# Kernel optimization log

Hardware: AMD Instinct MI355X
Metric: run time of the kernel (lower is better)

## Reference

```python
import jax, jax.numpy as jnp
import numpy as np

NUM_TOTAL = 150000
NUM_USER = 50000
NUM_ITEM = NUM_TOTAL - NUM_USER
D = 128
SOC_L = 2
CO_L = 2
NEG = 10
R = 0.7
E_SOC = 1600000
E_CO = 3200000
B = 512
MAX_UI = 64
MAX_IU = 50
W = 32
HOP = 3


def _sage_lgcn(x, src, dst, w, n, layers):
    # SAGEConv with edge-softmax weights over destination (LGCN 'mean' option).
    m = jax.lax.stop_gradient(jax.ops.segment_max(w, dst, num_segments=n))
    e = jnp.exp(w - m[dst])
    s = jax.ops.segment_sum(e, dst, num_segments=n)
    alpha = e / (s[dst] + 1e-16)
    for _ in range(layers):
        x = jax.ops.segment_sum(alpha[:, None] * x[src], dst, num_segments=n)
    return x  # LGCN.forward returns the last conv output (not the averaged sum)


def _sym_lgcn(x, src, dst, n, layers):
    # LGCConv: gcn_norm with added self-loops, symmetric D^-1/2 A D^-1/2.
    loop = jnp.arange(n)
    s2 = jnp.concatenate([src, loop])
    d2 = jnp.concatenate([dst, loop])
    deg = jax.ops.segment_sum(jnp.ones_like(d2, dtype=jnp.float32), d2, num_segments=n)
    dinv = jnp.where(deg > 0, deg ** -0.5, 0.0)
    ew = dinv[s2] * dinv[d2]
    for _ in range(layers):
        x = jax.ops.segment_sum(ew[:, None] * x[s2], d2, num_segments=n)
    return x


def _l2norm(x):
    return x / jnp.maximum(jnp.linalg.norm(x, axis=-1, keepdims=True), 1e-12)


def setup_inputs() -> dict:
    ks = jax.random.split(jax.random.key(0), 10)
    id_emb = 0.1 * jax.random.normal(ks[0], (NUM_TOTAL, D), jnp.float32)
    soc_id_emb = 0.1 * jax.random.normal(ks[1], (NUM_TOTAL, D), jnp.float32)
    soc_ext_weight = jax.random.uniform(ks[2], (E_SOC,), jnp.float32)
    soc_edge_index = jax.random.randint(ks[3], (2, E_SOC), 0, NUM_TOTAL)
    co_edge_index = jax.random.randint(ks[4], (2, E_CO), 0, NUM_TOTAL)
    uid = jax.random.randint(ks[5], (B,), 0, NUM_USER)
    pi = jax.random.randint(ks[9], (B,), NUM_USER, NUM_TOTAL)
    n_id = jnp.stack([uid, pi], axis=1)
    user_items = jax.random.randint(ks[6], (B, MAX_UI), 0, NUM_ITEM)
    item_users = jax.random.randint(ks[7], (NUM_ITEM, MAX_IU), 0, NUM_USER)
    walks = jax.random.randint(ks[8], (B, W, HOP), 0, NUM_TOTAL)
    return dict(id_emb=id_emb, soc_id_emb=soc_id_emb, soc_ext_weight=soc_ext_weight,
                soc_edge_index=soc_edge_index, co_edge_index=co_edge_index, n_id=n_id,
                user_items=user_items, item_users=item_users, walks=walks)


def reference(id_emb, soc_id_emb, soc_ext_weight, soc_edge_index, co_edge_index,
              n_id, user_items, item_users, walks):
    pi_id = n_id[:, 1]
    # two message-passing stacks
    soc_emb = _sage_lgcn(soc_id_emb, soc_edge_index[0], soc_edge_index[1],
                         soc_ext_weight, NUM_TOTAL, SOC_L)
    co_emb = _sym_lgcn(id_emb, co_edge_index[0], co_edge_index[1], NUM_TOTAL, CO_L)
    zero = jnp.zeros((1, D), id_emb.dtype)
    co_pad = jnp.concatenate([co_emb, zero], 0)
    soc_pad = jnp.concatenate([soc_emb, zero], 0)
    # vectorized per-user negative sampling: exclude interacted items, sample
    # NEG without replacement via top-k over masked uniform noise.
    rows = jnp.arange(B)[:, None]
    cols = jnp.where(user_items >= 0, user_items, 0)
    avail = jnp.ones((B, NUM_ITEM), jnp.int32).at[rows, cols].min(
        (user_items < 0).astype(jnp.int32))
    noise = jax.random.uniform(jax.random.key(42), (B, NUM_ITEM))
    scorez = jnp.where(avail > 0, noise, -1.0)
    _, neg_local = jax.lax.top_k(scorez, NEG)
    cand = jnp.concatenate([pi_id[:, None], neg_local + NUM_USER], axis=1)  # [B, 1+NEG]
    # item anchor soc embedding = mean of soc_emb over interacting users
    iu_idx = jnp.where(item_users >= 0, item_users, NUM_TOTAL)  # pad -> zero row
    cnt = (item_users >= 0).sum(-1, keepdims=True).astype(id_emb.dtype) + 1e-7
    anchor = soc_pad[iu_idx].sum(1) / cnt  # [NUM_ITEM, D]
    u_ref = jnp.concatenate([soc_emb[:NUM_USER], anchor, zero], 0)  # [NUM_TOTAL+1, D]
    co_n = _l2norm(co_pad)
    soc_n = _l2norm(u_ref)
    wk = walks.reshape(B, -1)  # [B, W*HOP]
    co_sim = (jnp.einsum('bcd,bwd->bcw', co_n[cand], co_n[wk]) + 1.0) * 0.5
    soc_sim = (jnp.einsum('bcd,bwd->bcw', soc_n[cand], soc_n[wk]) + 1.0) * 0.5
    return R * co_sim.mean(-1) + (1.0 - R) * soc_sim.mean(-1)  # [B, 1+NEG]
```

## Files before the change

### kernel.cpp

```cpp
#include <hip/hip_runtime.h>
#include <hip/hip_fp16.h>
#include <stdint.h>

#define NUM_TOTAL 150000
#define NUM_USER  50000
#define NUM_ITEM  100000
#define E_SOC 1600000
#define E_CO  3200000
#define BATCH 512
#define MAX_UI 64
#define MAX_IU 50
#define NWALK 96
#define NCAND 11
#define MASKW 3125
#define NB    586
#define NWG   192

__device__ __forceinline__ uint32_t rotl32(uint32_t x, int r){ return (x<<r)|(x>>(32-r)); }

__device__ __forceinline__ void tf_core(uint32_t x0, uint32_t x1, uint32_t& o0, uint32_t& o1){
  const uint32_t k0 = 0u, k1 = 42u, k2 = 0u ^ 42u ^ 0x1BD11BDAu;
  x0 += k0; x1 += k1;
#define TF_R4(a,b,c,d) \
  x0+=x1; x1=rotl32(x1,a); x1^=x0; \
  x0+=x1; x1=rotl32(x1,b); x1^=x0; \
  x0+=x1; x1=rotl32(x1,c); x1^=x0; \
  x0+=x1; x1=rotl32(x1,d); x1^=x0;
  TF_R4(13,15,26,6)   x0+=k1; x1+=k2+1u;
  TF_R4(17,29,16,24)  x0+=k2; x1+=k0+2u;
  TF_R4(13,15,26,6)   x0+=k0; x1+=k1+3u;
  TF_R4(17,29,16,24)  x0+=k1; x1+=k2+4u;
  TF_R4(13,15,26,6)   x0+=k2; x1+=k0+5u;
#undef TF_R4
  o0 = x0; o1 = x1;
}

__device__ __forceinline__ uint32_t tf_bits(uint32_t j){
  uint32_t o0, o1;
  tf_core(0u, j, o0, o1);
  return o0 ^ o1;
}

__global__ __launch_bounds__(256) void pcount_k(const int* __restrict__ dst, int E, int chunk,
                                                int* __restrict__ cntMat ){
  __shared__ int h[NB];
  int tid = threadIdx.x, wg = blockIdx.x;
  for (int i=tid; i<NB; i+=256) h[i]=0;
  __syncthreads();
  int lo = wg*chunk, hi = lo+chunk; if (hi > E) hi = E;
  for (int i=lo+tid; i<hi; i+=256) atomicAdd(&h[dst[i]>>8], 1);
  __syncthreads();
  for (int i=tid; i<NB; i+=256) cntMat[wg*NB + i] = h[i];
}

__global__ __launch_bounds__(1024) void pscan_k(int* __restrict__ cntMat, int* __restrict__ bbase, int E){
  __shared__ int sa[1024];
  int tid = threadIdx.x;
  int tot = 0;
  if (tid < NB){
    for (int wg=0; wg<NWG; ++wg) tot += cntMat[wg*NB + tid];
  }
  sa[tid] = tot;
  __syncthreads();
  for (int s=1; s<1024; s<<=1){
    int v = (tid>=s)?sa[tid-s]:0;
    __syncthreads();
    sa[tid] += v;
    __syncthreads();
  }
  if (tid < NB){
    int base = sa[tid] - tot;
    bbase[tid] = base;
    int run = base;
    for (int wg=0; wg<NWG; ++wg){
      int c = cntMat[wg*NB + tid];
      cntMat[wg*NB + tid] = run;
      run += c;
    }
  }
  if (tid == 0) bbase[NB] = E;
}

__global__ __launch_bounds__(256) void pplace_soc_k(const int* __restrict__ src,
        const int* __restrict__ dst, const float* __restrict__ wgt,
        const int* __restrict__ offMat, unsigned long long* __restrict__ rec, int E, int chunk){
  __shared__ int curx[NB];
  int tid = threadIdx.x, wg = blockIdx.x;
  for (int i=tid; i<NB; i+=256) curx[i] = offMat[wg*NB + i];
  __syncthreads();
  int lo = wg*chunk, hi = lo+chunk; if (hi > E) hi = E;
  for (int i=lo+tid; i<hi; i+=256){
    int d = dst[i];
    int p = atomicAdd(&curx[d>>8], 1);
    rec[p] = ((unsigned long long)__float_as_uint(wgt[i])<<32)
           | (unsigned)(((d&255)<<18) | src[i]);
  }
}

__global__ __launch_bounds__(256) void pplace_co_k(const int* __restrict__ src,
        const int* __restrict__ dst, const int* __restrict__ offMat,
        unsigned int* __restrict__ rec, int E, int chunk){
  __shared__ int curx[NB];
  int tid = threadIdx.x, wg = blockIdx.x;
  for (int i=tid; i<NB; i+=256) curx[i] = offMat[wg*NB + i];
  __syncthreads();
  int lo = wg*chunk, hi = lo+chunk; if (hi > E) hi = E;
  for (int i=lo+tid; i<hi; i+=256){
    int d = dst[i];
    int p = atomicAdd(&curx[d>>8], 1);
    rec[p] = (unsigned)(((d&255)<<18) | src[i]);
  }
}

__global__ __launch_bounds__(256) void csc_soc_k(const unsigned long long* __restrict__ rec,
    const int* __restrict__ bbase, int* __restrict__ off,
    int* __restrict__ srcS, float* __restrict__ wS){
  __shared__ int cnt[256], basex[256], curx[256];
  int b = blockIdx.x, tid = threadIdx.x;
  int lo = bbase[b], hi = bbase[b+1];
  cnt[tid] = 0;
  __syncthreads();
  for (int i = lo + tid; i < hi; i += 256){
    unsigned long long r = rec[i];
    atomicAdd(&cnt[(((unsigned)r) >> 18) & 255], 1);
  }
  __syncthreads();
  int c = cnt[tid];
  basex[tid] = c; __syncthreads();
  for (int s=1; s<256; s<<=1){
    int t = (tid>=s)?basex[tid-s]:0; __syncthreads();
    basex[tid]+=t; __syncthreads();
  }
  int excl = basex[tid]-c;
  int node = b*256+tid;
  if (node <= NUM_TOTAL) off[node] = lo + excl;
  basex[tid] = excl; curx[tid] = 0;
  __syncthreads();
  for (int i = lo + tid; i < hi; i += 256){
    unsigned long long r = rec[i];
    unsigned lw = (unsigned)r;
    int dl = (lw>>18)&255;
    int p = lo + basex[dl] + atomicAdd(&curx[dl],1);
    srcS[p] = lw & 0x3FFFF;
    wS[p] = __uint_as_float((unsigned)(r>>32));
  }
}

__global__ __launch_bounds__(256) void csc_co_k(const unsigned int* __restrict__ rec,
    const int* __restrict__ bbase, int* __restrict__ off, int* __restrict__ srcS){
  __shared__ int cnt[256], basex[256], curx[256];
  int b = blockIdx.x, tid = threadIdx.x;
  int lo = bbase[b], hi = bbase[b+1];
  cnt[tid] = 0;
  __syncthreads();
  for (int i = lo + tid; i < hi; i += 256){
    unsigned r = rec[i];
    atomicAdd(&cnt[(r >> 18) & 255], 1);
  }
  __syncthreads();
  int c = cnt[tid];
  basex[tid] = c; __syncthreads();
  for (int s=1; s<256; s<<=1){
    int t = (tid>=s)?basex[tid-s]:0; __syncthreads();
    basex[tid]+=t; __syncthreads();
  }
  int excl = basex[tid]-c;
  int node = b*256+tid;
  if (node <= NUM_TOTAL) off[node] = lo + excl;
  basex[tid] = excl; curx[tid] = 0;
  __syncthreads();
  for (int i = lo + tid; i < hi; i += 256){
    unsigned r = rec[i];
    int dl = (r>>18)&255;
    int p = lo + basex[dl] + atomicAdd(&curx[dl],1);
    srcS[p] = r & 0x3FFFF;
  }
}

__global__ void dinv_k(const int* __restrict__ off, float* __restrict__ dinv, int n){
  int i = blockIdx.x*blockDim.x + threadIdx.x, st = gridDim.x*blockDim.x;
  for (; i<n; i+=st){
    int deg = off[i+1]-off[i];
    dinv[i] = 1.0f / sqrtf((float)(deg + 1));
  }
}

__global__ void alpha_k(const int* __restrict__ off, float* __restrict__ wS, int n){
  int v = blockIdx.x*blockDim.x + threadIdx.x;
  if (v >= n) return;
  int e0 = off[v], e1 = off[v+1];
  if (e0 == e1) return;
  float m = -3.402823466e+38f;
  for (int e=e0; e<e1; ++e) m = fmaxf(m, wS[e]);
  float s = 0.f;
  for (int e=e0; e<e1; ++e) s += expf(wS[e] - m);
  float inv = 1.0f / (s + 1e-16f);
  for (int e=e0; e<e1; ++e) wS[e] = expf(wS[e] - m) * inv;
}

__global__ void f2h2_k(const float4* __restrict__ a, uint2* __restrict__ oa,
                       const float4* __restrict__ b, uint2* __restrict__ ob, int n4){
  int i = blockIdx.x*blockDim.x+threadIdx.x, st = gridDim.x*blockDim.x;
  for (; i<n4; i+=st){
    float4 va = a[i], vb = b[i];
    __half2 l = __float22half2_rn(make_float2(va.x,va.y));
    __half2 h = __float22half2_rn(make_float2(va.z,va.w));
    uint2 u; u.x = *(unsigned*)&l; u.y = *(unsigned*)&h;
    oa[i] = u;
    l = __float22half2_rn(make_float2(vb.x,vb.y));
    h = __float22half2_rn(make_float2(vb.z,vb.w));
    u.x = *(unsigned*)&l; u.y = *(unsigned*)&h;
    ob[i] = u;
  }
}

__global__ void agg_soc8_k(const __half2* __restrict__ x, __half2* __restrict__ y,
                           const int* __restrict__ off, const int* __restrict__ srcS,
                           const float* __restrict__ wE, int n){
  int gw = (blockIdx.x*blockDim.x + threadIdx.x) >> 6;
  int lane = threadIdx.x & 63;
  if (gw >= n) return;
  float ax = 0.f, ay = 0.f;
  int e = off[gw], e1 = off[gw+1];
  for (; e + 8 <= e1; e += 8){
    int s0=srcS[e],s1=srcS[e+1],s2=srcS[e+2],s3=srcS[e+3];
    int s4=srcS[e+4],s5=srcS[e+5],s6=srcS[e+6],s7=srcS[e+7];
    float a0=wE[e],a1=wE[e+1],a2=wE[e+2],a3=wE[e+3];
    float a4=wE[e+4],a5=wE[e+5],a6=wE[e+6],a7=wE[e+7];
    __half2 h0=x[(size_t)s0*64+lane], h1=x[(size_t)s1*64+lane];
    __half2 h2=x[(size_t)s2*64+lane], h3=x[(size_t)s3*64+lane];
    __half2 h4=x[(size_t)s4*64+lane], h5=x[(size_t)s5*64+lane];
    __half2 h6=x[(size_t)s6*64+lane], h7=x[(size_t)s7*64+lane];
    float2 f0=__half22float2(h0), f1=__half22float2(h1), f2=__half22float2(h2), f3=__half22float2(h3);
    float2 f4=__half22float2(h4), f5=__half22float2(h5), f6=__half22float2(h6), f7=__half22float2(h7);
    ax += a0*f0.x + a1*f1.x + a2*f2.x + a3*f3.x + a4*f4.x + a5*f5.x + a6*f6.x + a7*f7.x;
    ay += a0*f0.y + a1*f1.y + a2*f2.y + a3*f3.y + a4*f4.y + a5*f5.y + a6*f6.y + a7*f7.y;
  }
  for (; e < e1; ++e){
    int s = srcS[e]; float a = wE[e];
    float2 f = __half22float2(x[(size_t)s*64 + lane]);
    ax += a*f.x; ay += a*f.y;
  }
  y[(size_t)gw*64 + lane] = __float22half2_rn(make_float2(ax, ay));
}

__global__ void agg_co8_k(const __half2* __restrict__ x, __half2* __restrict__ y,
                          const int* __restrict__ off, const int* __restrict__ srcS,
                          const float* __restrict__ dinv, int n){
  int gw = (blockIdx.x*blockDim.x + threadIdx.x) >> 6;
  int lane = threadIdx.x & 63;
  if (gw >= n) return;
  float dv = dinv[gw];
  float2 fs = __half22float2(x[(size_t)gw*64 + lane]);
  float ax = dv*dv*fs.x, ay = dv*dv*fs.y;
  int e = off[gw], e1 = off[gw+1];
  for (; e + 8 <= e1; e += 8){
    int s0=srcS[e],s1=srcS[e+1],s2=srcS[e+2],s3=srcS[e+3];
    int s4=srcS[e+4],s5=srcS[e+5],s6=srcS[e+6],s7=srcS[e+7];
    float a0=dinv[s0]*dv,a1=dinv[s1]*dv,a2=dinv[s2]*dv,a3=dinv[s3]*dv;
    float a4=dinv[s4]*dv,a5=dinv[s5]*dv,a6=dinv[s6]*dv,a7=dinv[s7]*dv;
    __half2 h0=x[(size_t)s0*64+lane], h1=x[(size_t)s1*64+lane];
    __half2 h2=x[(size_t)s2*64+lane], h3=x[(size_t)s3*64+lane];
    __half2 h4=x[(size_t)s4*64+lane], h5=x[(size_t)s5*64+lane];
    __half2 h6=x[(size_t)s6*64+lane], h7=x[(size_t)s7*64+lane];
    float2 f0=__half22float2(h0), f1=__half22float2(h1), f2=__half22float2(h2), f3=__half22float2(h3);
    float2 f4=__half22float2(h4), f5=__half22float2(h5), f6=__half22float2(h6), f7=__half22float2(h7);
    ax += a0*f0.x + a1*f1.x + a2*f2.x + a3*f3.x + a4*f4.x + a5*f5.x + a6*f6.x + a7*f7.x;
    ay += a0*f0.y + a1*f1.y + a2*f2.y + a3*f3.y + a4*f4.y + a5*f5.y + a6*f6.y + a7*f7.y;
  }
  for (; e < e1; ++e){
    int s = srcS[e]; float a = dinv[s]*dv;
    float2 f = __half22float2(x[(size_t)s*64 + lane]);
    ax += a*f.x; ay += a*f.y;
  }
  y[(size_t)gw*64 + lane] = __float22half2_rn(make_float2(ax, ay));
}

__global__ void norm_h_k(__half2* __restrict__ x, int n){
  int gw = (blockIdx.x*blockDim.x + threadIdx.x) >> 6;
  int lane = threadIdx.x & 63;
  if (gw >= n) return;
  __half2* p = x + (size_t)gw*64;
  float2 v = __half22float2(p[lane]);
  float ss = v.x*v.x + v.y*v.y;
  #pragma unroll
  for (int s=32; s; s>>=1) ss += __shfl_xor(ss, s, 64);
  float sc = 1.0f / fmaxf(sqrtf(ss), 1e-12f);
  p[lane] = __float22half2_rn(make_float2(v.x*sc, v.y*sc));
}

__global__ void anchor_h_k(const __half2* __restrict__ soc, const int* __restrict__ item_users,
                           __half2* __restrict__ outI, int n){
  int gw = (blockIdx.x*blockDim.x + threadIdx.x) >> 6;
  int lane = threadIdx.x & 63;
  if (gw >= n) return;
  const int* us = item_users + (size_t)gw*MAX_IU;
  float ax = 0.f, ay = 0.f;
  for (int k=0; k<MAX_IU; k+=10){
    int u0=us[k],u1=us[k+1],u2=us[k+2],u3=us[k+3],u4=us[k+4];
    int u5=us[k+5],u6=us[k+6],u7=us[k+7],u8=us[k+8],u9=us[k+9];
    __half2 h0=soc[(size_t)u0*64+lane], h1=soc[(size_t)u1*64+lane];
    __half2 h2=soc[(size_t)u2*64+lane], h3=soc[(size_t)u3*64+lane];
    __half2 h4=soc[(size_t)u4*64+lane], h5=soc[(size_t)u5*64+lane];
    __half2 h6=soc[(size_t)u6*64+lane], h7=soc[(size_t)u7*64+lane];
    __half2 h8=soc[(size_t)u8*64+lane], h9=soc[(size_t)u9*64+lane];
    float2 f0=__half22float2(h0), f1=__half22float2(h1), f2=__half22float2(h2);
    float2 f3=__half22float2(h3), f4=__half22float2(h4), f5=__half22float2(h5);
    float2 f6=__half22float2(h6), f7=__half22float2(h7), f8=__half22float2(h8);
    float2 f9=__half22float2(h9);
    ax += f0.x+f1.x+f2.x+f3.x+f4.x+f5.x+f6.x+f7.x+f8.x+f9.x;
    ay += f0.y+f1.y+f2.y+f3.y+f4.y+f5.y+f6.y+f7.y+f8.y+f9.y;
  }
  const float inv = 1.0f / (50.0f + 1e-7f);
  ax *= inv; ay *= inv;
  float ss = ax*ax + ay*ay;
  #pragma unroll
  for (int s=32; s; s>>=1) ss += __shfl_xor(ss, s, 64);
  float sc = 1.0f / fmaxf(sqrtf(ss), 1e-12f);
  outI[(size_t)gw*64 + lane] = __float22half2_rn(make_float2(ax*sc, ay*sc));
}

__global__ __launch_bounds__(256) void topk_k(const int* __restrict__ user_items,
                                              const int* __restrict__ n_id,
                                              int* __restrict__ cand){
  __shared__ unsigned int mask[MASKW];
  __shared__ unsigned long long pool[2560];
  __shared__ unsigned long long red[256];
  int b = blockIdx.x, tid = threadIdx.x;
  for (int i=tid; i<MASKW; i+=256) mask[i] = 0u;
  __syncthreads();
  if (tid < MAX_UI){
    int it = user_items[b*MAX_UI + tid];
    if (it >= 0) atomicOr(&mask[it>>5], 1u << (it & 31));
  }
  __syncthreads();

  unsigned long long best[10];
  #pragma unroll
  for (int k=0; k<10; ++k) best[k] = 0ull;

  unsigned int jbase = (unsigned int)b * 100000u;
  for (int i=tid; i<NUM_ITEM; i+=256){
    if ((mask[i>>5] >> (i & 31)) & 1u) continue;
    unsigned int bits = tf_bits(jbase + (unsigned int)i);
    unsigned int v = bits >> 9;
    unsigned long long key = ((unsigned long long)v << 32) | (unsigned int)(~(unsigned int)i);
    if (key > best[9]){
      best[9] = key;
      #pragma unroll
      for (int r=9; r>0; --r)
        if (best[r] > best[r-1]){ unsigned long long t = best[r-1]; best[r-1] = best[r]; best[r] = t; }
    }
  }
  #pragma unroll
  for (int k=0; k<10; ++k) pool[tid*10 + k] = best[k];
  __syncthreads();

  for (int r=0; r<10; ++r){
    unsigned long long m = 0ull;
    #pragma unroll
    for (int k=0; k<10; ++k){ unsigned long long p = pool[tid*10 + k]; if (p > m) m = p; }
    red[tid] = m; __syncthreads();
    for (int s=128; s>0; s>>=1){
      if (tid < s && red[tid+s] > red[tid]) red[tid] = red[tid+s];
      __syncthreads();
    }
    unsigned long long win = red[0];
    if (tid == 0)
      cand[b*NCAND + 1 + r] = NUM_USER + (int)(~(unsigned int)(win & 0xffffffffull));
    #pragma unroll
    for (int k=0; k<10; ++k) if (pool[tid*10 + k] == win) pool[tid*10 + k] = 0ull;
    __syncthreads();
  }
  if (tid == 0) cand[b*NCAND] = n_id[b*2 + 1];
}

__global__ void sim_h_k(const __half2* __restrict__ coN, const __half2* __restrict__ socU,
                        const __half2* __restrict__ socI, const int* __restrict__ cand,
                        const int* __restrict__ walks, float* __restrict__ out){
  int b = blockIdx.x;
  int lane = threadIdx.x;
  float scx=0.f, scy=0.f, ssx=0.f, ssy=0.f;
  for (int w=0; w<NWALK; w+=4){
    int i0 = walks[b*NWALK + w],   i1 = walks[b*NWALK + w+1];
    int i2 = walks[b*NWALK + w+2], i3 = walks[b*NWALK + w+3];
    __half2 c0 = coN[(size_t)i0*64 + lane], c1 = coN[(size_t)i1*64 + lane];
    __half2 c2 = coN[(size_t)i2*64 + lane], c3 = coN[(size_t)i3*64 + lane];
    const __half2* p0 = (i0 < NUM_USER) ? socU + (size_t)i0*64 : socI + (size_t)(i0-NUM_USER)*64;
    const __half2* p1 = (i1 < NUM_USER) ? socU + (size_t)i1*64 : socI + (size_t)(i1-NUM_USER)*64;
    const __half2* p2 = (i2 < NUM_USER) ? socU + (size_t)i2*64 : socI + (size_t)(i2-NUM_USER)*64;
    const __half2* p3 = (i3 < NUM_USER) ? socU + (size_t)i3*64 : socI + (size_t)(i3-NUM_USER)*64;
    __half2 s0 = p0[lane], s1 = p1[lane], s2 = p2[lane], s3 = p3[lane];
    float2 fc0 = __half22float2(c0), fc1 = __half22float2(c1);
    float2 fc2 = __half22float2(c2), fc3 = __half22float2(c3);
    float2 fs0 = __half22float2(s0), fs1 = __half22float2(s1);
    float2 fs2 = __half22float2(s2), fs3 = __half22float2(s3);
    scx += fc0.x + fc1.x + fc2.x + fc3.x;
    scy += fc0.y + fc1.y + fc2.y + fc3.y;
    ssx += fs0.x + fs1.x + fs2.x + fs3.x;
    ssy += fs0.y + fs1.y + fs2.y + fs3.y;
  }
  for (int c=0; c<NCAND; ++c){
    int idx = cand[b*NCAND + c];
    float2 cv = __half22float2(coN[(size_t)idx*64 + lane]);
    float2 sv = __half22float2(socI[(size_t)(idx - NUM_USER)*64 + lane]);
    float dco = cv.x*scx + cv.y*scy;
    float dso = sv.x*ssx + sv.y*ssy;
    #pragma unroll
    for (int s=32; s; s>>=1){
      dco += __shfl_xor(dco, s, 64);
      dso += __shfl_xor(dso, s, 64);
    }
    if (lane == 0){
      float com = 0.5f + 0.5f*(dco / 96.0f);
      float som = 0.5f + 0.5f*(dso / 96.0f);
      out[b*NCAND + c] = 0.7f*com + 0.3f*som;
    }
  }
}

extern "C" void kernel_launch(void* const* d_in, const int* in_sizes, int n_in,
                              void* d_out, int out_size, void* d_ws, size_t ws_size,
                              hipStream_t stream){
  (void)in_sizes; (void)n_in; (void)out_size; (void)ws_size;
  const float* id_emb     = (const float*)d_in[0];
  const float* soc_id_emb = (const float*)d_in[1];
  const float* soc_w      = (const float*)d_in[2];
  const int*   soc_ei     = (const int*)d_in[3];
  const int*   co_ei      = (const int*)d_in[4];
  const int*   n_id       = (const int*)d_in[5];
  const int*   user_items = (const int*)d_in[6];
  const int*   item_users = (const int*)d_in[7];
  const int*   walks      = (const int*)d_in[8];
  float* out = (float*)d_out;

  char* w = (char*)d_ws;
  size_t cur = 0;
  auto take = [&](size_t bytes)->void*{
    void* p = w + cur;
    cur = (cur + bytes + 255) & ~(size_t)255;
    return p;
  };
  __half2* socId16 = (__half2*)take((size_t)NUM_TOTAL*64*4);
  __half2* id16    = (__half2*)take((size_t)NUM_TOTAL*64*4);
  __half2* t16     = (__half2*)take((size_t)NUM_TOTAL*64*4);
  __half2* soc16   = (__half2*)take((size_t)NUM_TOTAL*64*4);
  __half2* co16    = (__half2*)take((size_t)NUM_TOTAL*64*4);
  int*   socOff  = (int*)take((size_t)(NUM_TOTAL+1)*4);
  int*   coOff   = (int*)take((size_t)(NUM_TOTAL+1)*4);
  float* dinv    = (float*)take((size_t)NUM_TOTAL*4);
  int*   socSrcS = (int*)take((size_t)E_SOC*4);
  float* socWS   = (float*)take((size_t)E_SOC*4);
  int*   coSrcS  = (int*)take((size_t)E_CO*4);
  int*   cntMatS = (int*)take((size_t)NWG*NB*4);
  int*   cntMatC = (int*)take((size_t)NWG*NB*4);
  int*   bbaseS  = (int*)take((size_t)(NB+1)*4);
  int*   bbaseC  = (int*)take((size_t)(NB+1)*4);
  int*   cand    = (int*)take((size_t)BATCH*NCAND*4);

  unsigned long long* recS = (unsigned long long*)t16;
  unsigned int*       recC = (unsigned int*)((char*)t16 + (size_t)E_SOC*8);

  __half2* anch16 = socId16;

  const int T = 256;
  const int chunkS = (E_SOC + NWG - 1) / NWG;
  const int chunkC = (E_CO  + NWG - 1) / NWG;

  pcount_k<<<NWG, T, 0, stream>>>(soc_ei + E_SOC, E_SOC, chunkS, cntMatS);
  pcount_k<<<NWG, T, 0, stream>>>(co_ei + E_CO,  E_CO,  chunkC, cntMatC);
  pscan_k<<<1, 1024, 0, stream>>>(cntMatS, bbaseS, E_SOC);
  pscan_k<<<1, 1024, 0, stream>>>(cntMatC, bbaseC, E_CO);
  pplace_soc_k<<<NWG, T, 0, stream>>>(soc_ei, soc_ei + E_SOC, soc_w, cntMatS, recS, E_SOC, chunkS);
  pplace_co_k <<<NWG, T, 0, stream>>>(co_ei,  co_ei  + E_CO,         cntMatC, recC, E_CO,  chunkC);
  csc_soc_k<<<NB, T, 0, stream>>>(recS, bbaseS, socOff, socSrcS, socWS);
  csc_co_k <<<NB, T, 0, stream>>>(recC, bbaseC, coOff, coSrcS);

  dinv_k<<<(NUM_TOTAL + T - 1)/T, T, 0, stream>>>(coOff, dinv, NUM_TOTAL);
  alpha_k<<<(NUM_TOTAL + T - 1)/T, T, 0, stream>>>(socOff, socWS, NUM_TOTAL);

  f2h2_k<<<2048, T, 0, stream>>>((const float4*)soc_id_emb, (uint2*)socId16,
                                 (const float4*)id_emb,     (uint2*)id16, NUM_TOTAL*32);

  int aggGrid = (NUM_TOTAL + 3) / 4;
  agg_soc8_k<<<aggGrid, T, 0, stream>>>(socId16, soc16, socOff, socSrcS, socWS, NUM_TOTAL);
  agg_soc8_k<<<aggGrid, T, 0, stream>>>(soc16,   t16,   socOff, socSrcS, socWS, NUM_TOTAL);
  agg_co8_k <<<aggGrid, T, 0, stream>>>(id16,    co16,  coOff,  coSrcS,  dinv,  NUM_TOTAL);
  agg_co8_k <<<aggGrid, T, 0, stream>>>(co16,    id16,  coOff,  coSrcS,  dinv,  NUM_TOTAL);

  __half2* socE = t16;
  __half2* coE  = id16;

  norm_h_k<<<aggGrid, T, 0, stream>>>(coE, NUM_TOTAL);
  anchor_h_k<<<(NUM_ITEM + 3)/4, T, 0, stream>>>(socE, item_users, anch16, NUM_ITEM);
  norm_h_k<<<(NUM_USER + 3)/4, T, 0, stream>>>(socE, NUM_USER);

  topk_k<<<BATCH, T, 0, stream>>>(user_items, n_id, cand);
  sim_h_k<<<BATCH, 64, 0, stream>>>(coE, socE, anch16, cand, walks, out);
}
```

Baseline: 1.155 ms.

## Split negative top-k into threshold-filter pass and small merge pass

The per-row top-10 over 100k random scores is replaced by two kernels. The first spreads each row over four blocks, keeps only candidates whose score clears a fixed threshold, and writes them to a small survivor buffer. The second selects the top 10 from those survivors. If fewer than 10 survive, it falls back to a slow full rescan, so the result stays exact. This removes the per-thread insertion sort and serial reduction over 100k items, and uses more blocks for better parallelism. The threshold is tuned to the score distribution, and the survivor cap could overflow, so it depends on the noise statistics.

```diff
diff --git a/kernel.cpp b/kernel.cpp
--- a/kernel.cpp
+++ b/kernel.cpp
@@ -12,9 +12,13 @@
 #define MAX_IU 50
 #define NWALK 96
 #define NCAND 11
-#define MASKW 3125
 #define NB    586
 #define NWG   192
+#define PARTS 4
+#define PIT   25000
+#define PMW   784
+#define SCAP  192
+#define TH    8377900u
 
 __device__ __forceinline__ uint32_t rotl32(uint32_t x, int r){ return (x<<r)|(x>>(32-r)); }
 
@@ -320,57 +324,108 @@
   outI[(size_t)gw*64 + lane] = __float22half2_rn(make_float2(ax*sc, ay*sc));
 }
 
-__global__ __launch_bounds__(256) void topk_k(const int* __restrict__ user_items,
+__global__ __launch_bounds__(256) void negA_k(const int* __restrict__ user_items,
+                                              unsigned long long* __restrict__ surv,
+                                              int* __restrict__ scnt){
+  __shared__ unsigned int mask[PMW];
+  __shared__ int lcnt;
+  int blk = blockIdx.x;
+  int row = blk >> 2, part = blk & 3;
+  int base = part * PIT;
+  int tid = threadIdx.x;
+  for (int i=tid; i<PMW; i+=256) mask[i] = 0u;
+  if (tid == 0) lcnt = 0;
+  __syncthreads();
+  if (tid < MAX_UI){
+    int it = user_items[row*MAX_UI + tid];
+    if (it >= base && it < base + PIT){
+      int li = it - base;
+      atomicOr(&mask[li>>5], 1u << (li & 31));
+    }
+  }
+  __syncthreads();
+  unsigned jbase = (unsigned)row * 100000u + (unsigned)base;
+  for (int k = tid; k < PIT; k += 512){
+    int i1 = k + 256;
+    uint32_t b0 = tf_bits(jbase + (unsigned)k);
+    uint32_t b1 = tf_bits(jbase + (unsigned)(i1 < PIT ? i1 : k));
+    uint32_t v0 = b0 >> 9;
+    uint32_t v1 = b1 >> 9;
+    if (v0 >= TH && !((mask[k>>5] >> (k&31)) & 1u)){
+      int p = atomicAdd(&lcnt, 1);
+      if (p < SCAP)
+        surv[(size_t)blk*SCAP + p] = ((unsigned long long)v0 << 32) | (unsigned)(~(unsigned)(base + k));
+    }
+    if (i1 < PIT && v1 >= TH && !((mask[i1>>5] >> (i1&31)) & 1u)){
+      int p = atomicAdd(&lcnt, 1);
+      if (p < SCAP)
+        surv[(size_t)blk*SCAP + p] = ((unsigned long long)v1 << 32) | (unsigned)(~(unsigned)(base + i1));
+    }
+  }
+  __syncthreads();
+  if (tid == 0) scnt[blk] = (lcnt < SCAP) ? lcnt : SCAP;
+}
+
+__global__ __launch_bounds__(256) void negB_k(const unsigned long long* __restrict__ surv,
+                                              const int* __restrict__ scnt,
+                                              const int* __restrict__ user_items,
                                               const int* __restrict__ n_id,
                                               int* __restrict__ cand){
-  __shared__ unsigned int mask[MASKW];
-  __shared__ unsigned long long pool[2560];
+  __shared__ unsigned long long keys[PARTS*SCAP];
   __shared__ unsigned long long red[256];
+  __shared__ int cnts[PARTS];
+  __shared__ int uix[MAX_UI];
   int b = blockIdx.x, tid = threadIdx.x;
-  for (int i=tid; i<MASKW; i+=256) mask[i] = 0u;
-  __syncthreads();
-  if (tid < MAX_UI){
-    int it = user_items[b*MAX_UI + tid];
-    if (it >= 0) atomicOr(&mask[it>>5], 1u << (it & 31));
-  }
-  __syncthreads();
-
-  unsigned long long best[10];
-  #pragma unroll
-  for (int k=0; k<10; ++k) best[k] = 0ull;
-
-  unsigned int jbase = (unsigned int)b * 100000u;
-  for (int i=tid; i<NUM_ITEM; i+=256){
-    if ((mask[i>>5] >> (i & 31)) & 1u) continue;
-    unsigned int bits = tf_bits(jbase + (unsigned int)i);
-    unsigned int v = bits >> 9;
-    unsigned long long key = ((unsigned long long)v << 32) | (unsigned int)(~(unsigned int)i);
-    if (key > best[9]){
-      best[9] = key;
-      #pragma unroll
-      for (int r=9; r>0; --r)
-        if (best[r] > best[r-1]){ unsigned long long t = best[r-1]; best[r-1] = best[r]; best[r] = t; }
-    }
-  }
-  #pragma unroll
-  for (int k=0; k<10; ++k) pool[tid*10 + k] = best[k];
-  __syncthreads();
-
-  for (int r=0; r<10; ++r){
-    unsigned long long m = 0ull;
-    #pragma unroll
-    for (int k=0; k<10; ++k){ unsigned long long p = pool[tid*10 + k]; if (p > m) m = p; }
-    red[tid] = m; __syncthreads();
-    for (int s=128; s>0; s>>=1){
-      if (tid < s && red[tid+s] > red[tid]) red[tid] = red[tid+s];
+  if (tid < PARTS) cnts[tid] = scnt[b*PARTS + tid];
+  for (int i=tid; i<PARTS*SCAP; i+=256) keys[i] = 0ull;
+  __syncthreads();
+  int o0 = 0, o1 = cnts[0], o2 = o1 + cnts[1], o3 = o2 + cnts[2];
+  int total = o3 + cnts[3];
+  if (tid < cnts[0]) keys[o0 + tid] = surv[(size_t)(b*PARTS+0)*SCAP + tid];
+  if (tid < cnts[1]) keys[o1 + tid] = surv[(size_t)(b*PARTS+1)*SCAP + tid];
+  if (tid < cnts[2]) keys[o2 + tid] = surv[(size_t)(b*PARTS+2)*SCAP + tid];
+  if (tid < cnts[3]) keys[o3 + tid] = surv[(size_t)(b*PARTS+3)*SCAP + tid];
+  __syncthreads();
+  if (total >= 10){
+    for (int r=0; r<10; ++r){
+      unsigned long long m = 0ull;
+      for (int i=tid; i<PARTS*SCAP; i+=256){ unsigned long long v = keys[i]; if (v > m) m = v; }
+      red[tid] = m; __syncthreads();
+      for (int s=128; s>0; s>>=1){
+        if (tid < s && red[tid+s] > red[tid]) red[tid] = red[tid+s];
+        __syncthreads();
+      }
+      unsigned long long win = red[0];
+      if (tid == 0)
+        cand[b*NCAND + 1 + r] = NUM_USER + (int)(~(unsigned)(win & 0xffffffffull));
+      for (int i=tid; i<PARTS*SCAP; i+=256) if (keys[i] == win) keys[i] = 0ull;
       __syncthreads();
     }
-    unsigned long long win = red[0];
-    if (tid == 0)
-      cand[b*NCAND + 1 + r] = NUM_USER + (int)(~(unsigned int)(win & 0xffffffffull));
-    #pragma unroll
-    for (int k=0; k<10; ++k) if (pool[tid*10 + k] == win) pool[tid*10 + k] = 0ull;
+  } else {
+    if (tid < MAX_UI) uix[tid] = user_items[b*MAX_UI + tid];
     __syncthreads();
+    unsigned long long prev = ~0ull;
+    for (int r=0; r<10; ++r){
+      unsigned long long m = 0ull;
+      for (int i=tid; i<NUM_ITEM; i+=256){
+        bool msk = false;
+        for (int j=0; j<MAX_UI; ++j) if (uix[j] == i) msk = true;
+        if (msk) continue;
+        uint32_t v = tf_bits((unsigned)b*100000u + (unsigned)i) >> 9;
+        unsigned long long key = ((unsigned long long)v << 32) | (unsigned)(~(unsigned)i);
+        if (key < prev && key > m) m = key;
+      }
+      red[tid] = m; __syncthreads();
+      for (int s=128; s>0; s>>=1){
+        if (tid < s && red[tid+s] > red[tid]) red[tid] = red[tid+s];
+        __syncthreads();
+      }
+      unsigned long long win = red[0];
+      prev = win;
+      if (tid == 0)
+        cand[b*NCAND + 1 + r] = NUM_USER + (int)(~(unsigned)(win & 0xffffffffull));
+      __syncthreads();
+    }
   }
   if (tid == 0) cand[b*NCAND] = n_id[b*2 + 1];
 }
@@ -456,6 +511,8 @@
   int*   cntMatC = (int*)take((size_t)NWG*NB*4);
   int*   bbaseS  = (int*)take((size_t)(NB+1)*4);
   int*   bbaseC  = (int*)take((size_t)(NB+1)*4);
+  unsigned long long* surv = (unsigned long long*)take((size_t)BATCH*PARTS*SCAP*8);
+  int*   scnt    = (int*)take((size_t)BATCH*PARTS*4);
   int*   cand    = (int*)take((size_t)BATCH*NCAND*4);
 
   unsigned long long* recS = (unsigned long long*)t16;
@@ -479,6 +536,8 @@
   dinv_k<<<(NUM_TOTAL + T - 1)/T, T, 0, stream>>>(coOff, dinv, NUM_TOTAL);
   alpha_k<<<(NUM_TOTAL + T - 1)/T, T, 0, stream>>>(socOff, socWS, NUM_TOTAL);
 
+  negA_k<<<BATCH*PARTS, T, 0, stream>>>(user_items, surv, scnt);
+
   f2h2_k<<<2048, T, 0, stream>>>((const float4*)soc_id_emb, (uint2*)socId16,
                                  (const float4*)id_emb,     (uint2*)id16, NUM_TOTAL*32);
 
@@ -495,6 +554,6 @@
   anchor_h_k<<<(NUM_ITEM + 3)/4, T, 0, stream>>>(socE, item_users, anch16, NUM_ITEM);
   norm_h_k<<<(NUM_USER + 3)/4, T, 0, stream>>>(socE, NUM_USER);
 
-  topk_k<<<BATCH, T, 0, stream>>>(user_items, n_id, cand);
+  negB_k<<<BATCH, T, 0, stream>>>(surv, scnt, user_items, n_id, cand);
   sim_h_k<<<BATCH, 64, 0, stream>>>(coE, socE, anch16, cand, walks, out);
 }
```

Result: faster. 1.054 ms (-8.8%).
